# Performance work log

Hardware: AMD Instinct MI355X
Metric: run time of the kernel (lower is better)

The kernel has to match this reference:

```python
import jax, jax.numpy as jnp
import numpy as np

B, S, H = 4, 2048, 1024
E, K, INTER = 16, 2, 512
ALPHA, LIMIT = 1.702, 7.0


def setup_inputs() -> dict:
    key = jax.random.key(0)
    ks = jax.random.split(key, 6)
    return {
        "hidden_states": jax.random.normal(ks[0], (B, S, H), jnp.float32),
        "router_weight": jax.random.normal(ks[1], (H, E), jnp.float32) * 0.02,
        "gate_up_proj": jax.random.normal(ks[2], (E, H, 2 * INTER), jnp.float32) * 0.02,
        "gate_up_proj_bias": jax.random.normal(ks[3], (E, 2 * INTER), jnp.float32) * 0.02,
        "down_proj": jax.random.normal(ks[4], (E, INTER, H), jnp.float32) * 0.02,
        "down_proj_bias": jax.random.normal(ks[5], (E, H), jnp.float32) * 0.02,
    }


def reference(hidden_states, router_weight, gate_up_proj, gate_up_proj_bias,
              down_proj, down_proj_bias):
    b, s, h = hidden_states.shape
    x = hidden_states.reshape(-1, h)  # [T, H]
    # Router: linear logits -> top-k -> softmax over selected -> sparse scores [T, E]
    logits = x @ router_weight                      # [T, E]
    topk_w, topk_i = jax.lax.top_k(logits, K)       # [T, K]
    topk_w = jax.nn.softmax(topk_w, axis=-1)
    one_hot = (topk_i[..., None] == jnp.arange(E)[None, None, :]).astype(topk_w.dtype)
    scores = jnp.einsum('tk,tke->te', topk_w, one_hot)  # [T, E]
    # Fused gate+up projection per expert (num_devices=1 => dispatch/combine identity)
    gu = jnp.einsum('th,ehf->tef', x, gate_up_proj) + gate_up_proj_bias  # [T, E, 2I]
    gate = gu[..., ::2]   # interleaved layout
    up = gu[..., 1::2]
    # gpt_oss activation: clamp + scaled sigmoid glu
    gate = jnp.minimum(gate, LIMIT)
    up = jnp.clip(up, -LIMIT, LIMIT)
    glu = gate * jax.nn.sigmoid(gate * ALPHA)
    act = (up + 1.0) * glu                          # [T, E, I]
    # Down projection + score-weighted combine
    out = jnp.einsum('tei,eih,te->th', act, down_proj, scores)
    out = out + jnp.einsum('te,eh->th', scores, down_proj_bias)
    return out.reshape(b, s, h)
```

## Files before the change

kernel.cpp:

```cpp
#include <hip/hip_runtime.h>
#include <hip/hip_bf16.h>
#include <math.h>

#define TOK   8192
#define HDIM  1024
#define NE    16
#define NI    512
#define F2    1024
#define CAP   8192
#define CAP2  2048
#define ALPHA 1.702f
#define LIMIT 7.0f

typedef __attribute__((ext_vector_type(8))) short short8;
typedef __attribute__((ext_vector_type(4))) short short4v;
typedef __attribute__((ext_vector_type(4))) float f32x4;

static __device__ __forceinline__ unsigned short f2bf(float f) {
    unsigned int u = __float_as_uint(f);
    u += 0x7FFFu + ((u >> 16) & 1u);
    return (unsigned short)(u >> 16);
}
static __device__ __forceinline__ float bf2f(unsigned short u) {
    return __uint_as_float((unsigned int)u << 16);
}

#define GLD_LDS16(g, l) __builtin_amdgcn_global_load_lds(                     \
    (const __attribute__((address_space(1))) void*)(g),                       \
    (__attribute__((address_space(3))) void*)(l), 16, 0, 0)


static __device__ __forceinline__ void do_transpose(
    const float* __restrict__ in, unsigned short* __restrict__ out,
    int R, int C, int perm, int e, int bx, int by, char* smem, int tid)
{
    float (*t2)[65] = (float (*)[65])smem;
    const float* pin = in + (size_t)e * R * C;
    unsigned short* pout = out + (size_t)e * R * C;
    int c0 = bx * 64, r0 = by * 64;
#pragma unroll
    for (int j = 0; j < 4; ++j) {
        int idx4 = j * 256 + tid;
        int r = idx4 >> 4, c4 = (idx4 & 15) * 4;
        float4 v = *(const float4*)(pin + (size_t)(r0 + r) * C + c0 + c4);
        t2[c4 + 0][r] = v.x;
        t2[c4 + 1][r] = v.y;
        t2[c4 + 2][r] = v.z;
        t2[c4 + 3][r] = v.w;
    }
    __syncthreads();
#pragma unroll
    for (int j = 0; j < 2; ++j) {
        int idx = j * 256 + tid;
        int n = idx >> 3, k0 = (idx & 7) * 8;
        short8 v;
#pragma unroll
        for (int q = 0; q < 8; ++q) v[q] = (short)f2bf(t2[n][k0 + q]);
        int c = c0 + n;
        int orow;
        if (perm) {
            int tile = c >> 7, ct = c & 127;
            int fl = ct >> 1, h = ct & 1;
            orow = (tile << 7) | ((fl >> 4) << 5) | (h << 4) | (fl & 15);
        } else {
            orow = c;
        }
        *(short8*)(pout + (size_t)orow * R + r0 + k0) = v;
    }
}

__global__ __launch_bounds__(256) void prep_kernel(
    const float* __restrict__ x, const float* __restrict__ rw,
    const float* __restrict__ gup, const float* __restrict__ dwn,
    double* __restrict__ part, unsigned short* __restrict__ xbf,
    unsigned short* __restrict__ gupT, unsigned short* __restrict__ dwnT)
{
    __shared__ __align__(16) char smem[33792];
    int bid = blockIdx.x;
    int tid = threadIdx.x;

    if (bid < 4096) {
        do_transpose(gup, gupT, HDIM, F2, 1, bid >> 8, bid & 15, (bid >> 4) & 15, smem, tid);
        return;
    }
    if (bid < 6144) {
        int i = bid - 4096;
        do_transpose(dwn, dwnT, NI, HDIM, 0, i >> 7, i & 15, (i >> 4) & 7, smem, tid);
        return;
    }

    int idx = bid - 6144;
    int w = tid >> 6;
    int lane = tid & 63;
    int tt = lane & 15, eg = lane >> 4;
    int t0 = idx * 16;
    int hbase = w * 256;

    float* sx  = (float*)(smem + w * 8448);
    float* srw = (float*)(smem + w * 8448 + 4352);

    double acc[4] = {0.0, 0.0, 0.0, 0.0};

    for (int hc = 0; hc < 4; ++hc) {
        int h0 = hbase + hc * 64;
        __syncthreads();
#pragma unroll
        for (int j = 0; j < 4; ++j) {
            int fidx = j * 64 + lane;
            int t = fidx >> 4, c4 = (fidx & 15) * 4;
            float4 v = *(const float4*)(x + (size_t)(t0 + t) * HDIM + h0 + c4);
            *(float4*)&sx[t * 68 + c4] = v;
            short4v s;
            s[0] = (short)f2bf(v.x); s[1] = (short)f2bf(v.y);
            s[2] = (short)f2bf(v.z); s[3] = (short)f2bf(v.w);
            *(short4v*)(xbf + (size_t)(t0 + t) * HDIM + h0 + c4) = s;
        }
#pragma unroll
        for (int j = 0; j < 4; ++j) {
            int ridx = j * 64 + lane;
            int h = ridx >> 2, e4 = (ridx & 3) * 4;
            float4 v = *(const float4*)(rw + (size_t)(h0 + h) * NE + e4);
            *(float4*)&srw[h * 16 + e4] = v;
        }
        __syncthreads();
#pragma unroll 8
        for (int j = 0; j < 64; ++j) {
            float xv = sx[tt * 68 + j];
            float4 wv = *(const float4*)&srw[j * 16 + eg * 4];
            double xd = (double)xv;
            acc[0] += xd * (double)wv.x;
            acc[1] += xd * (double)wv.y;
            acc[2] += xd * (double)wv.z;
            acc[3] += xd * (double)wv.w;
        }
    }
#pragma unroll
    for (int q = 0; q < 4; ++q)
        part[(size_t)(w * NE + eg * 4 + q) * TOK + t0 + tt] = acc[q];
}

__global__ __launch_bounds__(256) void router_combine_kernel(
    const double* __restrict__ part,
    int* __restrict__ counts, int* __restrict__ toks, float* __restrict__ wgts,
    unsigned short* __restrict__ inv)
{
    __shared__ int lhist[NE];
    __shared__ int lbase[NE];
    int tid = threadIdx.x;
    int t = blockIdx.x * 256 + tid;
    if (tid < NE) lhist[tid] = 0;
    __syncthreads();

    double acc[NE];
#pragma unroll
    for (int e = 0; e < NE; ++e)
        acc[e] = part[(size_t)(0 * NE + e) * TOK + t]
               + part[(size_t)(1 * NE + e) * TOK + t]
               + part[(size_t)(2 * NE + e) * TOK + t]
               + part[(size_t)(3 * NE + e) * TOK + t];

    int i0 = 0; double v0 = acc[0];
#pragma unroll
    for (int e = 1; e < NE; ++e) if (acc[e] > v0) { v0 = acc[e]; i0 = e; }
    int i1 = -1; double v1 = -1e300;
#pragma unroll
    for (int e = 0; e < NE; ++e) if (e != i0 && acc[e] > v1) { v1 = acc[e]; i1 = e; }
    double e1 = exp(v1 - v0);
    float w0 = (float)(1.0 / (1.0 + e1));
    float w1 = (float)(e1 / (1.0 + e1));

    int r0 = atomicAdd(&lhist[i0], 1);
    int r1 = atomicAdd(&lhist[i1], 1);
    __syncthreads();
    if (tid < NE) lbase[tid] = atomicAdd(&counts[tid], lhist[tid]);
    __syncthreads();
    int p0 = lbase[i0] + r0; if (p0 > 2047) p0 = 2047;
    int p1 = lbase[i1] + r1; if (p1 > 2047) p1 = 2047;
    toks[i0 * CAP + p0] = t; wgts[i0 * CAP + p0] = w0;
    toks[i1 * CAP + p1] = t; wgts[i1 * CAP + p1] = w1;
    inv[2 * t]     = (unsigned short)((i0 << 11) | p0);
    inv[2 * t + 1] = (unsigned short)((i1 << 11) | p1);
}

#define KLOOP_BODY(NT, KOFF)                                                          \
    int c0 = 0;                                                                       \
    for (int kb = 0; kb < (NT); ++kb) {                                               \
        if (kb + 2 < (NT)) {                                                          \
            int cpre = c0 + 2; if (cpre >= 3) cpre -= 3;                              \
            _Pragma("unroll")                                                         \
            for (int i = 0; i < 2; ++i) {                                             \
                GLD_LDS16(gaA[i] + (kb + 2) * (KOFF), &As[cpre][w * 32 + i * 16][0]); \
                GLD_LDS16(gaB[i] + (kb + 2) * (KOFF), &Bs[cpre][w * 32 + i * 16][0]); \
            }                                                                         \
            asm volatile("s_waitcnt vmcnt(8)" ::: "memory");                          \
        } else if (kb + 1 < (NT)) {                                                   \
            asm volatile("s_waitcnt vmcnt(4)" ::: "memory");                          \
        } else {                                                                      \
            asm volatile("s_waitcnt vmcnt(0)" ::: "memory");                          \
        }                                                                             \
        __builtin_amdgcn_sched_barrier(0);                                            \
        __builtin_amdgcn_s_barrier();                                                 \
        __builtin_amdgcn_sched_barrier(0);                                            \
        short8 af[4], bfr[4];                                                         \
        _Pragma("unroll")                                                             \
        for (int m = 0; m < 4; ++m) af[m] = *(const short8*)&As[c0][wr * 64 + m * 16 + lr][slt]; \
        _Pragma("unroll")                                                             \
        for (int n = 0; n < 4; ++n) bfr[n] = *(const short8*)&Bs[c0][wc * 64 + n * 16 + lr][slt]; \
        _Pragma("unroll")                                                             \
        for (int m = 0; m < 4; ++m)                                                   \
            _Pragma("unroll")                                                         \
            for (int n = 0; n < 4; ++n)                                               \
                acc[m][n] = __builtin_amdgcn_mfma_f32_16x16x32_bf16(af[m], bfr[n], acc[m][n], 0, 0, 0); \
        asm volatile("s_waitcnt lgkmcnt(0)" ::: "memory");                            \
        __builtin_amdgcn_sched_barrier(0);                                            \
        __builtin_amdgcn_s_barrier();                                                 \
        __builtin_amdgcn_sched_barrier(0);                                            \
        c0 = (c0 + 1 == 3) ? 0 : c0 + 1;                                              \
    }

#define KLOOP_PROLOGUE(KOFF)                                                          \
    _Pragma("unroll")                                                                 \
    for (int i = 0; i < 2; ++i) {                                                     \
        GLD_LDS16(gaA[i], &As[0][w * 32 + i * 16][0]);                                \
        GLD_LDS16(gaB[i], &Bs[0][w * 32 + i * 16][0]);                                \
    }                                                                                 \
    _Pragma("unroll")                                                                 \
    for (int i = 0; i < 2; ++i) {                                                     \
        GLD_LDS16(gaA[i] + (KOFF), &As[1][w * 32 + i * 16][0]);                       \
        GLD_LDS16(gaB[i] + (KOFF), &Bs[1][w * 32 + i * 16][0]);                       \
    }

__global__ __launch_bounds__(256) void gemm1_kernel(
    const unsigned short* __restrict__ xb, const unsigned short* __restrict__ gupT,
    const float* __restrict__ gub,
    const int* __restrict__ counts, const int* __restrict__ toks,
    unsigned short* __restrict__ act, const unsigned short* __restrict__ zp)
{
    int b = blockIdx.x;
    int e = b & 15;
    int j = b >> 4;
    int nt = j & 7;
    int mt = j >> 3;
    int cnt = counts[e];
    int row0 = mt * 128;
    if (row0 >= cnt) return;
    int n0 = nt * 128;

    __shared__ __align__(16) unsigned short As[3][128][32];
    __shared__ __align__(16) unsigned short Bs[3][128][32];
    __shared__ int rtok[128];

    int tid = threadIdx.x;
    int lane = tid & 63;
    int w = tid >> 6;
    int wr = w >> 1, wc = w & 1;
    int lr = lane & 15, lg = lane >> 4;

    if (tid < 128) {
        int p = row0 + tid;
        rtok[tid] = (p < cnt) ? toks[e * CAP + p] : -1;
    }
    __syncthreads();

    int srow = lane >> 2;
    int scol = (((lane & 3) ^ ((lane >> 3) & 3)) * 8);
    int slt = (lg ^ ((lr >> 1) & 3)) * 8;

    const unsigned short* gaA[2];
    const unsigned short* gaB[2];
    const unsigned short* gupE = gupT + (size_t)e * HDIM * F2;
#pragma unroll
    for (int i = 0; i < 2; ++i) {
        int arow = w * 32 + i * 16 + srow;
        int tk = rtok[arow];
        gaA[i] = (tk >= 0) ? (xb + (size_t)tk * HDIM + scol) : (zp + scol);
        int brow = n0 + w * 32 + i * 16 + srow;
        gaB[i] = gupE + (size_t)brow * HDIM + scol;
    }

    f32x4 acc[4][4];
#pragma unroll
    for (int m = 0; m < 4; ++m)
#pragma unroll
        for (int n = 0; n < 4; ++n) acc[m][n] = (f32x4){0.f, 0.f, 0.f, 0.f};

    KLOOP_PROLOGUE(32)
    KLOOP_BODY(HDIM / 32, 32)

    unsigned short* actE = act + (size_t)e * CAP2 * NI;
    int fbase = nt * 64 + wc * 32;
#pragma unroll
    for (int q = 0; q < 2; ++q) {
        int f = fbase + q * 16 + lr;
        float bg = gub[e * F2 + 2 * f];
        float bu = gub[e * F2 + 2 * f + 1];
#pragma unroll
        for (int m = 0; m < 4; ++m) {
#pragma unroll
            for (int r = 0; r < 4; ++r) {
                float gate = acc[m][2 * q][r] + bg;
                float up   = acc[m][2 * q + 1][r] + bu;
                gate = fminf(gate, LIMIT);
                up   = fminf(fmaxf(up, -LIMIT), LIMIT);
                float glu = gate / (1.0f + __expf(-ALPHA * gate));
                float av  = (up + 1.0f) * glu;
                int row = row0 + wr * 64 + m * 16 + lg * 4 + r;
                actE[(size_t)row * NI + f] = f2bf(av);
            }
        }
    }
}

__global__ __launch_bounds__(256) void gemm2_y_kernel(
    const unsigned short* __restrict__ act, const unsigned short* __restrict__ dwnT,
    const float* __restrict__ dwb,
    const int* __restrict__ counts, const float* __restrict__ wgts,
    unsigned short* __restrict__ y)
{
    int b = blockIdx.x;
    int e = b & 15;
    int j = b >> 4;
    int nt = j & 7;
    int mt = j >> 3;
    int cnt = counts[e];
    int row0 = mt * 128;
    if (row0 >= cnt) return;
    int n0 = nt * 128;

    int base_e = 0;
#pragma unroll
    for (int q = 0; q < NE; ++q) base_e += (q < e) ? counts[q] : 0;

    __shared__ __align__(16) unsigned short As[3][128][32];
    __shared__ __align__(16) unsigned short Bs[3][128][32];
    __shared__ float rwgt[128];

    int tid = threadIdx.x;
    int lane = tid & 63;
    int w = tid >> 6;
    int wr = w >> 1, wc = w & 1;
    int lr = lane & 15, lg = lane >> 4;

    if (tid < 128) {
        int p = row0 + tid;
        rwgt[tid] = (p < cnt) ? wgts[e * CAP + p] : 0.0f;
    }
    __syncthreads();

    int srow = lane >> 2;
    int scol = (((lane & 3) ^ ((lane >> 3) & 3)) * 8);
    int slt = (lg ^ ((lr >> 1) & 3)) * 8;

    const unsigned short* gaA[2];
    const unsigned short* gaB[2];
    const unsigned short* actE = act + (size_t)e * CAP2 * NI;
    const unsigned short* dwnE = dwnT + (size_t)e * HDIM * NI;
#pragma unroll
    for (int i = 0; i < 2; ++i) {
        int arow = row0 + w * 32 + i * 16 + srow;
        gaA[i] = actE + (size_t)arow * NI + scol;
        int brow = n0 + w * 32 + i * 16 + srow;
        gaB[i] = dwnE + (size_t)brow * NI + scol;
    }

    f32x4 acc[4][4];
#pragma unroll
    for (int m = 0; m < 4; ++m)
#pragma unroll
        for (int n = 0; n < 4; ++n) acc[m][n] = (f32x4){0.f, 0.f, 0.f, 0.f};

    KLOOP_PROLOGUE(32)
    KLOOP_BODY(NI / 32, 32)

    unsigned short* yB = y + (size_t)(base_e + row0) * HDIM;
#pragma unroll
    for (int n = 0; n < 4; ++n) {
        int hc = n0 + wc * 64 + n * 16 + lr;
        float db = dwb[e * HDIM + hc];
#pragma unroll
        for (int m = 0; m < 4; ++m) {
#pragma unroll
            for (int r = 0; r < 4; ++r) {
                int rl = wr * 64 + m * 16 + lg * 4 + r;
                if (row0 + rl < cnt)
                    yB[(size_t)rl * HDIM + hc] = f2bf(rwgt[rl] * (acc[m][n][r] + db));
            }
        }
    }
}

__global__ __launch_bounds__(256) void out_combine_kernel(
    const unsigned short* __restrict__ y, const unsigned short* __restrict__ inv,
    const int* __restrict__ counts, float* __restrict__ out)
{
    __shared__ int sbase[NE];
    int tid = threadIdx.x;
    int t = blockIdx.x;
    if (tid == 0) {
        int s = 0;
#pragma unroll
        for (int e = 0; e < NE; ++e) { sbase[e] = s; s += counts[e]; }
    }
    __syncthreads();
    unsigned short v0 = inv[2 * t], v1 = inv[2 * t + 1];
    int s0 = sbase[v0 >> 11] + (v0 & 2047);
    int s1 = sbase[v1 >> 11] + (v1 & 2047);
    short4v a = *(const short4v*)(y + (size_t)s0 * HDIM + tid * 4);
    short4v c = *(const short4v*)(y + (size_t)s1 * HDIM + tid * 4);
    float4 o;
    o.x = bf2f((unsigned short)a[0]) + bf2f((unsigned short)c[0]);
    o.y = bf2f((unsigned short)a[1]) + bf2f((unsigned short)c[1]);
    o.z = bf2f((unsigned short)a[2]) + bf2f((unsigned short)c[2]);
    o.w = bf2f((unsigned short)a[3]) + bf2f((unsigned short)c[3]);
    *(float4*)(out + (size_t)t * HDIM + tid * 4) = o;
}

__global__ __launch_bounds__(256) void router_kernel(
    const float* __restrict__ x, const float* __restrict__ rw,
    int* __restrict__ counts, int* __restrict__ toks, float* __restrict__ wgts)
{
    int gwave = (int)((blockIdx.x * 256 + threadIdx.x) >> 6);
    int lane = threadIdx.x & 63;
    if (gwave >= TOK) return;
    const float* xr = x + (size_t)gwave * HDIM;
    double acc[NE];
#pragma unroll
    for (int e = 0; e < NE; ++e) acc[e] = 0.0;
    for (int i = 0; i < HDIM / 64; ++i) {
        int h = i * 64 + lane;
        double xv = (double)xr[h];
        const float* r = rw + (size_t)h * NE;
#pragma unroll
        for (int e = 0; e < NE; ++e) acc[e] += xv * (double)r[e];
    }
#pragma unroll
    for (int e = 0; e < NE; ++e) {
        double v = acc[e];
#pragma unroll
        for (int off = 32; off > 0; off >>= 1) v += __shfl_xor(v, off);
        acc[e] = v;
    }
    if (lane == 0) {
        int i0 = 0; double v0 = acc[0];
#pragma unroll
        for (int e = 1; e < NE; ++e) if (acc[e] > v0) { v0 = acc[e]; i0 = e; }
        int i1 = -1; double v1 = -1e300;
#pragma unroll
        for (int e = 0; e < NE; ++e) if (e != i0 && acc[e] > v1) { v1 = acc[e]; i1 = e; }
        double e1 = exp(v1 - v0);
        float w0 = (float)(1.0 / (1.0 + e1));
        float w1 = (float)(e1 / (1.0 + e1));
        int p0 = atomicAdd(&counts[i0], 1);
        toks[i0 * CAP + p0] = gwave; wgts[i0 * CAP + p0] = w0;
        int p1 = atomicAdd(&counts[i1], 1);
        toks[i1 * CAP + p1] = gwave; wgts[i1 * CAP + p1] = w1;
    }
}

__global__ __launch_bounds__(256) void moe_kernel(
    const float* __restrict__ x,
    const float* __restrict__ gup, const float* __restrict__ gub,
    const float* __restrict__ dwn, const float* __restrict__ dwb,
    const int* __restrict__ counts, const int* __restrict__ toks,
    const float* __restrict__ wgts, float* __restrict__ out)
{
    int e = blockIdx.y;
    int cnt = counts[e];
    int row0 = blockIdx.x * 64;
    if (row0 >= cnt) return;

    __shared__ __align__(16) unsigned short sA[64][40];
    __shared__ __align__(16) unsigned short sB[64][40];
    __shared__ __align__(16) unsigned short sAct[64][520];
    __shared__ int   rtok[64];
    __shared__ float rwgt[64];

    int tid = threadIdx.x;
    if (tid < 64) {
        int idx = row0 + tid;
        bool v = idx < cnt;
        rtok[tid] = v ? toks[e * CAP + idx] : -1;
        rwgt[tid] = v ? wgts[e * CAP + idx] : 0.0f;
    }
    __syncthreads();

    int lane = tid & 63;
    int w = tid >> 6;
    int wr = w >> 1, wc = w & 1;
    int lr = lane & 15, lg = lane >> 4;
    int ar = tid >> 2, ac0 = (tid & 3) * 8;
    int bk = tid >> 3, bf0 = (tid & 7) * 8;
    const float* gupE = gup + (size_t)e * HDIM * F2;

    for (int nb = 0; nb < F2 / 64; ++nb) {
        f32x4 acc[2][2];
#pragma unroll
        for (int mi = 0; mi < 2; ++mi)
#pragma unroll
            for (int ni = 0; ni < 2; ++ni) acc[mi][ni] = (f32x4){0.f, 0.f, 0.f, 0.f};
        for (int kb = 0; kb < HDIM / 32; ++kb) {
            __syncthreads();
            {
                int tk = rtok[ar];
                short8 vv = {0,0,0,0,0,0,0,0};
                if (tk >= 0) {
                    const float* p = x + (size_t)tk * HDIM + kb * 32 + ac0;
                    float4 u0 = *(const float4*)(p); float4 u1 = *(const float4*)(p + 4);
                    vv[0]=(short)f2bf(u0.x); vv[1]=(short)f2bf(u0.y); vv[2]=(short)f2bf(u0.z); vv[3]=(short)f2bf(u0.w);
                    vv[4]=(short)f2bf(u1.x); vv[5]=(short)f2bf(u1.y); vv[6]=(short)f2bf(u1.z); vv[7]=(short)f2bf(u1.w);
                }
                *(short8*)&sA[ar][ac0] = vv;
            }
            {
                const float* p = gupE + (size_t)(kb * 32 + bk) * F2 + nb * 64 + bf0;
                float4 u0 = *(const float4*)(p); float4 u1 = *(const float4*)(p + 4);
                sB[bf0+0][bk]=f2bf(u0.x); sB[bf0+1][bk]=f2bf(u0.y); sB[bf0+2][bk]=f2bf(u0.z); sB[bf0+3][bk]=f2bf(u0.w);
                sB[bf0+4][bk]=f2bf(u1.x); sB[bf0+5][bk]=f2bf(u1.y); sB[bf0+6][bk]=f2bf(u1.z); sB[bf0+7][bk]=f2bf(u1.w);
            }
            __syncthreads();
            short8 a0 = *(const short8*)&sA[wr*32+lr][lg*8];
            short8 a1 = *(const short8*)&sA[wr*32+16+lr][lg*8];
            short8 b0 = *(const short8*)&sB[wc*32+lr][lg*8];
            short8 b1 = *(const short8*)&sB[wc*32+16+lr][lg*8];
            acc[0][0] = __builtin_amdgcn_mfma_f32_16x16x32_bf16(a0,b0,acc[0][0],0,0,0);
            acc[0][1] = __builtin_amdgcn_mfma_f32_16x16x32_bf16(a0,b1,acc[0][1],0,0,0);
            acc[1][0] = __builtin_amdgcn_mfma_f32_16x16x32_bf16(a1,b0,acc[1][0],0,0,0);
            acc[1][1] = __builtin_amdgcn_mfma_f32_16x16x32_bf16(a1,b1,acc[1][1],0,0,0);
        }
#pragma unroll
        for (int ni = 0; ni < 2; ++ni) {
            int fc = nb * 64 + wc * 32 + ni * 16 + lr;
            float bias = gub[e * F2 + fc];
#pragma unroll
            for (int mi = 0; mi < 2; ++mi)
#pragma unroll
                for (int r = 0; r < 4; ++r) {
                    float gu = acc[mi][ni][r] + bias;
                    float other = __shfl_xor(gu, 1);
                    float gate = (lr & 1) ? other : gu;
                    float up   = (lr & 1) ? gu : other;
                    gate = fminf(gate, LIMIT);
                    up = fminf(fmaxf(up, -LIMIT), LIMIT);
                    float glu = gate / (1.0f + __expf(-ALPHA * gate));
                    float av = (up + 1.0f) * glu;
                    if (!(lr & 1)) sAct[wr*32+mi*16+lg*4+r][fc >> 1] = f2bf(av);
                }
        }
    }
    __syncthreads();

    const float* dwnE = dwn + (size_t)e * NI * HDIM;
    int tks[2][4]; float wvs[2][4];
#pragma unroll
    for (int mi = 0; mi < 2; ++mi)
#pragma unroll
        for (int r = 0; r < 4; ++r) {
            int row = wr*32 + mi*16 + lg*4 + r;
            tks[mi][r] = rtok[row]; wvs[mi][r] = rwgt[row];
        }
    for (int nb = 0; nb < HDIM / 64; ++nb) {
        f32x4 acc[2][2];
#pragma unroll
        for (int mi = 0; mi < 2; ++mi)
#pragma unroll
            for (int ni = 0; ni < 2; ++ni) acc[mi][ni] = (f32x4){0.f,0.f,0.f,0.f};
        for (int kb = 0; kb < NI / 32; ++kb) {
            __syncthreads();
            {
                const float* p = dwnE + (size_t)(kb*32 + bk) * HDIM + nb*64 + bf0;
                float4 u0 = *(const float4*)(p); float4 u1 = *(const float4*)(p + 4);
                sB[bf0+0][bk]=f2bf(u0.x); sB[bf0+1][bk]=f2bf(u0.y); sB[bf0+2][bk]=f2bf(u0.z); sB[bf0+3][bk]=f2bf(u0.w);
                sB[bf0+4][bk]=f2bf(u1.x); sB[bf0+5][bk]=f2bf(u1.y); sB[bf0+6][bk]=f2bf(u1.z); sB[bf0+7][bk]=f2bf(u1.w);
            }
            __syncthreads();
            short8 a0 = *(const short8*)&sAct[wr*32+lr][kb*32+lg*8];
            short8 a1 = *(const short8*)&sAct[wr*32+16+lr][kb*32+lg*8];
            short8 b0 = *(const short8*)&sB[wc*32+lr][lg*8];
            short8 b1 = *(const short8*)&sB[wc*32+16+lr][lg*8];
            acc[0][0] = __builtin_amdgcn_mfma_f32_16x16x32_bf16(a0,b0,acc[0][0],0,0,0);
            acc[0][1] = __builtin_amdgcn_mfma_f32_16x16x32_bf16(a0,b1,acc[0][1],0,0,0);
            acc[1][0] = __builtin_amdgcn_mfma_f32_16x16x32_bf16(a1,b0,acc[1][0],0,0,0);
            acc[1][1] = __builtin_amdgcn_mfma_f32_16x16x32_bf16(a1,b1,acc[1][1],0,0,0);
        }
#pragma unroll
        for (int ni = 0; ni < 2; ++ni) {
            int hc = nb*64 + wc*32 + ni*16 + lr;
            float db = dwb[e * HDIM + hc];
#pragma unroll
            for (int mi = 0; mi < 2; ++mi)
#pragma unroll
                for (int r = 0; r < 4; ++r) {
                    int tk = tks[mi][r];
                    if (tk >= 0)
                        atomicAdd(out + (size_t)tk * HDIM + hc, wvs[mi][r] * (acc[mi][ni][r] + db));
                }
        }
    }
}

extern "C" void kernel_launch(void* const* d_in, const int* in_sizes, int n_in,
                              void* d_out, int out_size, void* d_ws, size_t ws_size,
                              hipStream_t stream) {
    const float* x   = (const float*)d_in[0];
    const float* rw  = (const float*)d_in[1];
    const float* gup = (const float*)d_in[2];
    const float* gub = (const float*)d_in[3];
    const float* dwn = (const float*)d_in[4];
    const float* dwb = (const float*)d_in[5];
    float* out = (float*)d_out;

    const size_t OFF_COUNTS = 0;
    const size_t OFF_ZP     = 256;
    const size_t OFF_INV    = 4352;
    const size_t OFF_TOKS   = OFF_INV  + (size_t)TOK * 2 * 2;
    const size_t OFF_WGTS   = OFF_TOKS + (size_t)NE * CAP * 4;
    const size_t OFF_DWNT   = OFF_WGTS + (size_t)NE * CAP * 4;
    const size_t OFF_ACT    = OFF_DWNT + (size_t)NE * NI * HDIM * 2;
    const size_t OFF_XBF    = OFF_ACT  + (size_t)NE * CAP2 * NI * 2;
    const size_t OFF_GUPT   = OFF_XBF  + (size_t)TOK * HDIM * 2;
    const size_t REQ_B      = OFF_GUPT + (size_t)NE * HDIM * F2 * 2;
    const size_t OFF_Y      = OFF_XBF;
    const size_t REQ_A      = OFF_Y + (size_t)2 * TOK * HDIM * 2;

    if (ws_size >= REQ_B) {
        int*            counts = (int*)((char*)d_ws + OFF_COUNTS);
        unsigned short* zp     = (unsigned short*)((char*)d_ws + OFF_ZP);
        unsigned short* inv    = (unsigned short*)((char*)d_ws + OFF_INV);
        int*            toks   = (int*)((char*)d_ws + OFF_TOKS);
        float*          wgts   = (float*)((char*)d_ws + OFF_WGTS);
        unsigned short* dwnT   = (unsigned short*)((char*)d_ws + OFF_DWNT);
        unsigned short* act    = (unsigned short*)((char*)d_ws + OFF_ACT);
        double*         part   = (double*)((char*)d_ws + OFF_ACT);
        unsigned short* xbf    = (unsigned short*)((char*)d_ws + OFF_XBF);
        unsigned short* gupT   = (unsigned short*)((char*)d_ws + OFF_GUPT);
        unsigned short* y      = (unsigned short*)((char*)d_ws + OFF_Y);

        hipMemsetAsync(d_ws, 0, 4352, stream);

        prep_kernel<<<4096 + 2048 + 512, 256, 0, stream>>>(
            x, rw, gup, dwn, part, xbf, gupT, dwnT);

        router_combine_kernel<<<TOK / 256, 256, 0, stream>>>(part, counts, toks, wgts, inv);

        int g1 = (CAP2 / 128) * (F2 / 128) * NE;
        gemm1_kernel<<<g1, 256, 0, stream>>>(xbf, gupT, gub, counts, toks, act, zp);
        int g2 = (CAP2 / 128) * (HDIM / 128) * NE;

        if (ws_size >= REQ_A) {
            gemm2_y_kernel<<<g2, 256, 0, stream>>>(act, dwnT, dwb, counts, wgts, y);
            out_combine_kernel<<<TOK, 256, 0, stream>>>(y, inv, counts, out);
        } else {
            hipMemsetAsync(d_out, 0, (size_t)out_size * sizeof(float), stream);
            out_combine_kernel<<<TOK, 256, 0, stream>>>(y, inv, counts, out);
        }
    } else {
        int*   counts = (int*)d_ws;
        int*   toks   = (int*)((char*)d_ws + 64);
        float* wgts   = (float*)((char*)d_ws + 64 + (size_t)NE * CAP * sizeof(int));
        hipMemsetAsync(d_ws, 0, 64, stream);
        hipMemsetAsync(d_out, 0, (size_t)out_size * sizeof(float), stream);
        router_kernel<<<TOK / 4, 256, 0, stream>>>(x, rw, counts, toks, wgts);
        dim3 gm(TOK / 64, NE);
        moe_kernel<<<gm, 256, 0, stream>>>(x, gup, gub, dwn, dwb, counts, toks, wgts, out);
    }
}
```

Baseline: 166.5 us.

## Convert to bf16 before LDS transpose and enlarge transpose tiles to 256 rows

```diff
diff --git a/kernel.cpp b/kernel.cpp
--- a/kernel.cpp
+++ b/kernel.cpp
@@ -30,32 +30,38 @@
     (__attribute__((address_space(3))) void*)(l), 16, 0, 0)
 
 
-static __device__ __forceinline__ void do_transpose(
+static __device__ __forceinline__ void do_transpose256(
     const float* __restrict__ in, unsigned short* __restrict__ out,
     int R, int C, int perm, int e, int bx, int by, char* smem, int tid)
 {
-    float (*t2)[65] = (float (*)[65])smem;
+    unsigned short (*t2)[264] = (unsigned short (*)[264])smem;
     const float* pin = in + (size_t)e * R * C;
     unsigned short* pout = out + (size_t)e * R * C;
-    int c0 = bx * 64, r0 = by * 64;
-#pragma unroll
-    for (int j = 0; j < 4; ++j) {
-        int idx4 = j * 256 + tid;
-        int r = idx4 >> 4, c4 = (idx4 & 15) * 4;
-        float4 v = *(const float4*)(pin + (size_t)(r0 + r) * C + c0 + c4);
-        t2[c4 + 0][r] = v.x;
-        t2[c4 + 1][r] = v.y;
-        t2[c4 + 2][r] = v.z;
-        t2[c4 + 3][r] = v.w;
-    }
-    __syncthreads();
-#pragma unroll
-    for (int j = 0; j < 2; ++j) {
+    int c0 = bx * 64, r0 = by * 256;
+
+#pragma unroll
+    for (int j = 0; j < 8; ++j) {
         int idx = j * 256 + tid;
-        int n = idx >> 3, k0 = (idx & 7) * 8;
-        short8 v;
-#pragma unroll
-        for (int q = 0; q < 8; ++q) v[q] = (short)f2bf(t2[n][k0 + q]);
+        int rp = idx >> 4, c4 = (idx & 15) * 4;
+        const float* p0 = pin + (size_t)(r0 + 2 * rp) * C + c0 + c4;
+        float4 v0 = *(const float4*)(p0);
+        float4 v1 = *(const float4*)(p0 + C);
+        unsigned int u0 = (unsigned int)f2bf(v0.x) | ((unsigned int)f2bf(v1.x) << 16);
+        unsigned int u1 = (unsigned int)f2bf(v0.y) | ((unsigned int)f2bf(v1.y) << 16);
+        unsigned int u2 = (unsigned int)f2bf(v0.z) | ((unsigned int)f2bf(v1.z) << 16);
+        unsigned int u3 = (unsigned int)f2bf(v0.w) | ((unsigned int)f2bf(v1.w) << 16);
+        *(unsigned int*)&t2[c4 + 0][2 * rp] = u0;
+        *(unsigned int*)&t2[c4 + 1][2 * rp] = u1;
+        *(unsigned int*)&t2[c4 + 2][2 * rp] = u2;
+        *(unsigned int*)&t2[c4 + 3][2 * rp] = u3;
+    }
+    __syncthreads();
+
+#pragma unroll
+    for (int j = 0; j < 8; ++j) {
+        int idx = j * 256 + tid;
+        int n = idx >> 5, k0 = (idx & 31) * 8;
+        short8 v = *(const short8*)&t2[n][k0];
         int c = c0 + n;
         int orow;
         if (perm) {
@@ -79,17 +85,18 @@
     int bid = blockIdx.x;
     int tid = threadIdx.x;
 
-    if (bid < 4096) {
-        do_transpose(gup, gupT, HDIM, F2, 1, bid >> 8, bid & 15, (bid >> 4) & 15, smem, tid);
+    if (bid >= 512) {
+        if (bid < 1536) {
+            int i = bid - 512;
+            do_transpose256(gup, gupT, HDIM, F2, 1, i >> 6, i & 15, (i >> 4) & 3, smem, tid);
+        } else {
+            int i = bid - 1536;
+            do_transpose256(dwn, dwnT, NI, HDIM, 0, i >> 5, i & 15, (i >> 4) & 1, smem, tid);
+        }
         return;
     }
-    if (bid < 6144) {
-        int i = bid - 4096;
-        do_transpose(dwn, dwnT, NI, HDIM, 0, i >> 7, i & 15, (i >> 4) & 7, smem, tid);
-        return;
-    }
-
-    int idx = bid - 6144;
+
+    int idx = bid;
     int w = tid >> 6;
     int lane = tid & 63;
     int tt = lane & 15, eg = lane >> 4;
@@ -637,7 +644,7 @@
 
         hipMemsetAsync(d_ws, 0, 4352, stream);
 
-        prep_kernel<<<4096 + 2048 + 512, 256, 0, stream>>>(
+        prep_kernel<<<512 + 1024 + 512, 256, 0, stream>>>(
             x, rw, gup, dwn, part, xbf, gupT, dwnT);
 
         router_combine_kernel<<<TOK / 256, 256, 0, stream>>>(part, counts, toks, wgts, inv);
```

New measurement: 159.9 us. 4.0% less time.
